# Performance work log

Hardware: AMD Instinct MI355X
Metric: run time of the kernel (lower is better)

## Reference

```python
import jax, jax.numpy as jnp
import numpy as np

B = 16384          # batch
NS = 26            # sparse features
ND = 13            # dense features
V = 100000         # vocab per sparse feature
E = 16             # embedding size
H = 400            # dnn hidden
DNN_IN = NS * E + ND  # 429


def setup_inputs() -> dict:
    key = jax.random.key(0)
    ks = jax.random.split(key, 12)
    X_sparse = jax.random.randint(ks[0], (B, NS), 0, V, dtype=jnp.int32)
    X_dense = jax.random.normal(ks[1], (B, ND), dtype=jnp.float32)
    # stacked per-feature embedding tables: [NS, V, dim]
    emb1 = jax.random.normal(ks[2], (NS, V, 1), dtype=jnp.float32) * 1e-4
    emb2 = jax.random.normal(ks[3], (NS, V, E), dtype=jnp.float32) * 1e-4
    lin_weight = jax.random.normal(ks[4], (ND, 1), dtype=jnp.float32) * 1e-4
    bias = jnp.zeros((1,), dtype=jnp.float32)
    W0 = jax.random.normal(ks[5], (DNN_IN, H), dtype=jnp.float32) * 1e-4
    b0 = jnp.zeros((H,), dtype=jnp.float32)
    W1 = jax.random.normal(ks[6], (H, H), dtype=jnp.float32) * 1e-4
    b1 = jnp.zeros((H,), dtype=jnp.float32)
    W2 = jax.random.normal(ks[7], (H, H), dtype=jnp.float32) * 1e-4
    b2 = jnp.zeros((H,), dtype=jnp.float32)
    W_out = jax.random.normal(ks[8], (H, 1), dtype=jnp.float32) * 1e-4
    return {"X_sparse": X_sparse, "X_dense": X_dense, "emb1": emb1, "emb2": emb2,
            "lin_weight": lin_weight, "bias": bias, "W0": W0, "b0": b0,
            "W1": W1, "b1": b1, "W2": W2, "b2": b2, "W_out": W_out}


def reference(X_sparse, X_dense, emb1, emb2, lin_weight, bias, W0, b0, W1, b1, W2, b2, W_out):
    fidx = jnp.arange(NS)[None, :]            # [1, NS] feature indices
    # ---- FM linear term ----
    e1 = emb1[fidx, X_sparse][..., 0]          # [B, NS] per-feature scalar embeddings
    linear_sparse = jnp.sum(e1, axis=-1, keepdims=True)            # [B, 1]
    linear_dense = X_dense @ lin_weight                            # [B, 1]
    logit = linear_sparse + linear_dense
    # ---- FM second-order cross term ----
    e2 = emb2[fidx, X_sparse]                  # [B, NS, E]
    square_of_sum = jnp.square(jnp.sum(e2, axis=1))                # [B, E]
    sum_of_square = jnp.sum(jnp.square(e2), axis=1)                # [B, E]
    cross = 0.5 * jnp.sum(square_of_sum - sum_of_square, axis=-1, keepdims=True)
    logit = logit + cross
    # ---- DNN (dropout p=0 -> identity) ----
    dnn_in = jnp.concatenate([e2.reshape(e2.shape[0], -1), X_dense], axis=-1)  # [B, 429]
    h = jax.nn.relu(dnn_in @ W0 + b0)
    h = jax.nn.relu(h @ W1 + b1)
    h = jax.nn.relu(h @ W2 + b2)
    logit = logit + h @ W_out
    return logit + bias
```

## Files before the change

### kernel.cpp

```cpp
#include <hip/hip_runtime.h>
#include <hip/hip_bf16.h>

#define B_     16384
#define NS_    26
#define ND_    13
#define V_     100000
#define E_     16
#define H_     400
#define HP     416
#define K0P    448

typedef __bf16 bf16x8 __attribute__((ext_vector_type(8)));
typedef float  f32x4  __attribute__((ext_vector_type(4)));

__device__ __forceinline__ unsigned short f2bf(float f) {
  __hip_bfloat16 h = __float2bfloat16(f);
  return __builtin_bit_cast(unsigned short, h);
}
__device__ __forceinline__ float bf2f(unsigned short u) {
  unsigned v = ((unsigned)u) << 16;
  return __builtin_bit_cast(float, v);
}

__global__ __launch_bounds__(256) void fm_kernel(
    const int* __restrict__ Xs, const float* __restrict__ Xd,
    const float* __restrict__ emb1, const float* __restrict__ emb2,
    const float* __restrict__ linw, const float* __restrict__ bias,
    unsigned short* __restrict__ dnn, float* __restrict__ out) {
  const int row  = blockIdx.x * 16 + (threadIdx.x >> 4);
  const int lane = threadIdx.x & 15;
  const int* xs = Xs + row * NS_;
  unsigned short* drow = dnn + (size_t)row * K0P;

  float s_sum = 0.f, s_sq = 0.f;
#pragma unroll
  for (int f = 0; f < NS_; ++f) {
    int idx = xs[f];
    float v = emb2[((size_t)f * V_ + idx) * E_ + lane];
    s_sum += v;
    s_sq  += v * v;
    drow[f * 16 + lane] = f2bf(v);
  }

  float lin = 0.f;
  for (int f = lane; f < NS_; f += 16)
    lin += emb1[(size_t)f * V_ + xs[f]];

  float xdv = 0.f;
  if (lane < ND_) {
    xdv = Xd[row * ND_ + lane];
    lin += xdv * linw[lane];
  }
  drow[416 + lane] = f2bf(lane < ND_ ? xdv : 0.f);
  drow[432 + lane] = 0;

  float r = 0.5f * (s_sum * s_sum - s_sq) + lin;
#pragma unroll
  for (int m = 8; m >= 1; m >>= 1) r += __shfl_xor(r, m, 64);
  if (lane == 0) out[row] = r + bias[0];
}

__global__ __launch_bounds__(256) void conv_w(
    const float* __restrict__ W, unsigned short* __restrict__ Wt, int K, int Kp) {
  int i = blockIdx.x * 256 + threadIdx.x;
  int total = Kp * HP;
  if (i >= total) return;
  int k = i / HP;
  int n = i - k * HP;
  float v = (k < K && n < H_) ? W[k * H_ + n] : 0.f;
  Wt[(size_t)n * Kp + k] = f2bf(v);
}

__global__ void pad_bias(const float* __restrict__ b, float* __restrict__ bp) {
  int i = blockIdx.x * 256 + threadIdx.x;
  if (i < HP) bp[i] = (i < H_) ? b[i] : 0.f;
}

__global__ __launch_bounds__(256) void gemm_relu(
    const unsigned short* __restrict__ A, const unsigned short* __restrict__ Bt,
    const float* __restrict__ bias, unsigned short* __restrict__ C, int K) {
  __shared__ unsigned short As[64][40];
  __shared__ unsigned short Bs[32][40];

  const int tid  = threadIdx.x;
  const int wave = tid >> 6;
  const int lane = tid & 63;
  const int quad = lane >> 4;
  const int l16  = lane & 15;
  const int rowBase = blockIdx.x * 64;
  const int colBase = blockIdx.y * 32;

  const int ar = tid >> 2, aseg = tid & 3;
  const int bn = tid >> 3, bseg = tid & 7;

  const unsigned short* aptr = A  + (size_t)(rowBase + ar) * K + aseg * 8;
  const unsigned short* bptr = Bt + (size_t)(colBase + bn) * K + bseg * 4;

  f32x4 acc0 = {0.f, 0.f, 0.f, 0.f};
  f32x4 acc1 = {0.f, 0.f, 0.f, 0.f};

  const int nK = K >> 5;
  for (int kt = 0; kt < nK; ++kt) {
    uint4 av = *(const uint4*)(aptr + kt * 32);
    uint2 bv = *(const uint2*)(bptr + kt * 32);
    __syncthreads();
    *(uint4*)&As[ar][aseg * 8] = av;
    *(uint2*)&Bs[bn][bseg * 4] = bv;
    __syncthreads();

    uint4 au  = *(const uint4*)&As[wave * 16 + l16][quad * 8];
    uint4 b0u = *(const uint4*)&Bs[l16][quad * 8];
    uint4 b1u = *(const uint4*)&Bs[16 + l16][quad * 8];
    bf16x8 af  = __builtin_bit_cast(bf16x8, au);
    bf16x8 bf0 = __builtin_bit_cast(bf16x8, b0u);
    bf16x8 bf1 = __builtin_bit_cast(bf16x8, b1u);
    acc0 = __builtin_amdgcn_mfma_f32_16x16x32_bf16(af, bf0, acc0, 0, 0, 0);
    acc1 = __builtin_amdgcn_mfma_f32_16x16x32_bf16(af, bf1, acc1, 0, 0, 0);
  }

#pragma unroll
  for (int t = 0; t < 2; ++t) {
    f32x4 a = (t == 0) ? acc0 : acc1;
    int col = colBase + t * 16 + l16;
    float bz = bias[col];
#pragma unroll
    for (int r = 0; r < 4; ++r) {
      int row = rowBase + wave * 16 + quad * 4 + r;
      float v = a[r] + bz;
      v = v > 0.f ? v : 0.f;
      C[(size_t)row * HP + col] = f2bf(v);
    }
  }
}

__global__ __launch_bounds__(256) void out_dot(
    const unsigned short* __restrict__ h2, const float* __restrict__ Wout,
    float* __restrict__ out) {
  const int row  = blockIdx.x * 4 + (threadIdx.x >> 6);
  const int lane = threadIdx.x & 63;
  const unsigned short* hr = h2 + (size_t)row * HP;
  float s = 0.f;
  for (int c = lane; c < H_; c += 64) s += bf2f(hr[c]) * Wout[c];
#pragma unroll
  for (int m = 32; m >= 1; m >>= 1) s += __shfl_xor(s, m, 64);
  if (lane == 0) out[row] += s;
}

extern "C" void kernel_launch(void* const* d_in, const int* in_sizes, int n_in,
                              void* d_out, int out_size, void* d_ws, size_t ws_size,
                              hipStream_t stream) {
  const int*   Xs   = (const int*)d_in[0];
  const float* Xd   = (const float*)d_in[1];
  const float* emb1 = (const float*)d_in[2];
  const float* emb2 = (const float*)d_in[3];
  const float* linw = (const float*)d_in[4];
  const float* bias = (const float*)d_in[5];
  const float* W0   = (const float*)d_in[6];
  const float* b0   = (const float*)d_in[7];
  const float* W1   = (const float*)d_in[8];
  const float* b1   = (const float*)d_in[9];
  const float* W2   = (const float*)d_in[10];
  const float* b2   = (const float*)d_in[11];
  const float* Wout = (const float*)d_in[12];
  float* out = (float*)d_out;

  char* ws = (char*)d_ws;
  unsigned short* P0  = (unsigned short*)(ws);
  unsigned short* P1  = (unsigned short*)(ws + 14680064);
  unsigned short* W0t = (unsigned short*)(ws + 28311552);
  unsigned short* W1t = (unsigned short*)(ws + 28684288);
  unsigned short* W2t = (unsigned short*)(ws + 29030400);
  float* b0p = (float*)(ws + 29376512);
  float* b1p = (float*)(ws + 29378176);
  float* b2p = (float*)(ws + 29379840);

  fm_kernel<<<B_ / 16, 256, 0, stream>>>(Xs, Xd, emb1, emb2, linw, bias, P0, out);

  conv_w<<<(K0P * HP + 255) / 256, 256, 0, stream>>>(W0, W0t, 429, K0P);
  conv_w<<<(HP * HP + 255) / 256, 256, 0, stream>>>(W1, W1t, 400, HP);
  conv_w<<<(HP * HP + 255) / 256, 256, 0, stream>>>(W2, W2t, 400, HP);
  pad_bias<<<2, 256, 0, stream>>>(b0, b0p);
  pad_bias<<<2, 256, 0, stream>>>(b1, b1p);
  pad_bias<<<2, 256, 0, stream>>>(b2, b2p);

  dim3 grid(B_ / 64, HP / 32);
  gemm_relu<<<grid, 256, 0, stream>>>(P0, W0t, b0p, P1, K0P);
  gemm_relu<<<grid, 256, 0, stream>>>(P1, W1t, b1p, P0, HP);
  gemm_relu<<<grid, 256, 0, stream>>>(P0, W2t, b2p, P1, HP);

  out_dot<<<B_ / 4, 256, 0, stream>>>(P1, Wout, out);
}
```

Baseline: 332.1 us.

## Enlarge GEMM tiles, prefetch operands, fuse output dot, merge weight conversion

The GEMM block tile grows from 64x32 to 128x64, with each wave computing a 32x64 sub-tile using eight MFMA accumulators, and the next k-slice is loaded from global memory into registers while the current one is computed. The last layer folds the Wout dot product into its epilogue with shuffle reductions and atomicAdd, so the final activation is never written and no separate out_dot kernel runs. The three weight conversions and the bias/Wout padding are merged into a single launch, and all padding is now 448. These changes cut launch count, global traffic and operand reloads, at the cost of more registers per thread, extra padded columns, and atomic contention on out.

```diff
diff --git a/kernel.cpp b/kernel.cpp
--- a/kernel.cpp
+++ b/kernel.cpp
@@ -7,8 +7,8 @@
 #define V_     100000
 #define E_     16
 #define H_     400
-#define HP     416
-#define K0P    448
+#define NP     448
+#define K0A    429
 
 typedef __bf16 bf16x8 __attribute__((ext_vector_type(8)));
 typedef float  f32x4  __attribute__((ext_vector_type(4)));
@@ -16,10 +16,6 @@
 __device__ __forceinline__ unsigned short f2bf(float f) {
   __hip_bfloat16 h = __float2bfloat16(f);
   return __builtin_bit_cast(unsigned short, h);
-}
-__device__ __forceinline__ float bf2f(unsigned short u) {
-  unsigned v = ((unsigned)u) << 16;
-  return __builtin_bit_cast(float, v);
 }
 
 __global__ __launch_bounds__(256) void fm_kernel(
@@ -30,7 +26,7 @@
   const int row  = blockIdx.x * 16 + (threadIdx.x >> 4);
   const int lane = threadIdx.x & 15;
   const int* xs = Xs + row * NS_;
-  unsigned short* drow = dnn + (size_t)row * K0P;
+  unsigned short* drow = dnn + (size_t)row * NP;
 
   float s_sum = 0.f, s_sq = 0.f;
 #pragma unroll
@@ -60,90 +56,124 @@
   if (lane == 0) out[row] = r + bias[0];
 }
 
-__global__ __launch_bounds__(256) void conv_w(
-    const float* __restrict__ W, unsigned short* __restrict__ Wt, int K, int Kp) {
+__global__ __launch_bounds__(256) void conv_all(
+    const float* __restrict__ W0, const float* __restrict__ W1,
+    const float* __restrict__ W2, const float* __restrict__ b0,
+    const float* __restrict__ b1, const float* __restrict__ b2,
+    const float* __restrict__ Wout,
+    unsigned short* __restrict__ W0t, unsigned short* __restrict__ W1t,
+    unsigned short* __restrict__ W2t, float* __restrict__ b0p,
+    float* __restrict__ b1p, float* __restrict__ b2p,
+    float* __restrict__ woutp) {
+  const int WSZ = NP * NP;
   int i = blockIdx.x * 256 + threadIdx.x;
-  int total = Kp * HP;
-  if (i >= total) return;
-  int k = i / HP;
-  int n = i - k * HP;
-  float v = (k < K && n < H_) ? W[k * H_ + n] : 0.f;
-  Wt[(size_t)n * Kp + k] = f2bf(v);
-}
-
-__global__ void pad_bias(const float* __restrict__ b, float* __restrict__ bp) {
-  int i = blockIdx.x * 256 + threadIdx.x;
-  if (i < HP) bp[i] = (i < H_) ? b[i] : 0.f;
+  if (i < 3 * WSZ) {
+    int which = i / WSZ;
+    int j = i - which * WSZ;
+    int k = j / NP, n = j - (j / NP) * NP;
+    const float* W = (which == 0) ? W0 : (which == 1) ? W1 : W2;
+    unsigned short* Wt = (which == 0) ? W0t : (which == 1) ? W1t : W2t;
+    int Kact = (which == 0) ? K0A : H_;
+    float v = (k < Kact && n < H_) ? W[k * H_ + n] : 0.f;
+    Wt[(size_t)n * NP + k] = f2bf(v);
+  } else {
+    int j = i - 3 * WSZ;
+    if (j < NP)          b0p[j]            = (j < H_) ? b0[j] : 0.f;
+    else if (j < 2 * NP) b1p[j - NP]       = (j - NP < H_) ? b1[j - NP] : 0.f;
+    else if (j < 3 * NP) b2p[j - 2 * NP]   = (j - 2 * NP < H_) ? b2[j - 2 * NP] : 0.f;
+    else if (j < 4 * NP) woutp[j - 3 * NP] = (j - 3 * NP < H_) ? Wout[j - 3 * NP] : 0.f;
+  }
 }
 
 __global__ __launch_bounds__(256) void gemm_relu(
     const unsigned short* __restrict__ A, const unsigned short* __restrict__ Bt,
-    const float* __restrict__ bias, unsigned short* __restrict__ C, int K) {
-  __shared__ unsigned short As[64][40];
-  __shared__ unsigned short Bs[32][40];
+    const float* __restrict__ bias, unsigned short* __restrict__ C,
+    const float* __restrict__ wout, float* __restrict__ out, int fuse) {
+  __shared__ unsigned short As[128][40];
+  __shared__ unsigned short Bs[64][40];
 
   const int tid  = threadIdx.x;
   const int wave = tid >> 6;
   const int lane = tid & 63;
   const int quad = lane >> 4;
   const int l16  = lane & 15;
-  const int rowBase = blockIdx.x * 64;
-  const int colBase = blockIdx.y * 32;
-
-  const int ar = tid >> 2, aseg = tid & 3;
-  const int bn = tid >> 3, bseg = tid & 7;
-
-  const unsigned short* aptr = A  + (size_t)(rowBase + ar) * K + aseg * 8;
-  const unsigned short* bptr = Bt + (size_t)(colBase + bn) * K + bseg * 4;
-
-  f32x4 acc0 = {0.f, 0.f, 0.f, 0.f};
-  f32x4 acc1 = {0.f, 0.f, 0.f, 0.f};
-
-  const int nK = K >> 5;
+  const int rowBase = blockIdx.x * 128;
+  const int colBase = blockIdx.y * 64;
+
+  const int sr = tid >> 2, sseg = tid & 3;
+  const unsigned short* aptr0 = A  + (size_t)(rowBase + sr) * NP + sseg * 8;
+  const unsigned short* aptr1 = A  + (size_t)(rowBase + 64 + sr) * NP + sseg * 8;
+  const unsigned short* bptr  = Bt + (size_t)(colBase + sr) * NP + sseg * 8;
+
+  f32x4 acc[2][4] = {};
+
+  uint4 a0 = *(const uint4*)(aptr0);
+  uint4 a1 = *(const uint4*)(aptr1);
+  uint4 bv = *(const uint4*)(bptr);
+
+  const int nK = NP / 32;
   for (int kt = 0; kt < nK; ++kt) {
-    uint4 av = *(const uint4*)(aptr + kt * 32);
-    uint2 bv = *(const uint2*)(bptr + kt * 32);
     __syncthreads();
-    *(uint4*)&As[ar][aseg * 8] = av;
-    *(uint2*)&Bs[bn][bseg * 4] = bv;
+    *(uint4*)&As[sr][sseg * 8]      = a0;
+    *(uint4*)&As[64 + sr][sseg * 8] = a1;
+    *(uint4*)&Bs[sr][sseg * 8]      = bv;
     __syncthreads();
 
-    uint4 au  = *(const uint4*)&As[wave * 16 + l16][quad * 8];
-    uint4 b0u = *(const uint4*)&Bs[l16][quad * 8];
-    uint4 b1u = *(const uint4*)&Bs[16 + l16][quad * 8];
-    bf16x8 af  = __builtin_bit_cast(bf16x8, au);
-    bf16x8 bf0 = __builtin_bit_cast(bf16x8, b0u);
-    bf16x8 bf1 = __builtin_bit_cast(bf16x8, b1u);
-    acc0 = __builtin_amdgcn_mfma_f32_16x16x32_bf16(af, bf0, acc0, 0, 0, 0);
-    acc1 = __builtin_amdgcn_mfma_f32_16x16x32_bf16(af, bf1, acc1, 0, 0, 0);
-  }
-
-#pragma unroll
-  for (int t = 0; t < 2; ++t) {
-    f32x4 a = (t == 0) ? acc0 : acc1;
-    int col = colBase + t * 16 + l16;
-    float bz = bias[col];
-#pragma unroll
-    for (int r = 0; r < 4; ++r) {
-      int row = rowBase + wave * 16 + quad * 4 + r;
-      float v = a[r] + bz;
-      v = v > 0.f ? v : 0.f;
-      C[(size_t)row * HP + col] = f2bf(v);
-    }
-  }
-}
-
-__global__ __launch_bounds__(256) void out_dot(
-    const unsigned short* __restrict__ h2, const float* __restrict__ Wout,
-    float* __restrict__ out) {
-  const int row  = blockIdx.x * 4 + (threadIdx.x >> 6);
-  const int lane = threadIdx.x & 63;
-  const unsigned short* hr = h2 + (size_t)row * HP;
-  float s = 0.f;
-  for (int c = lane; c < H_; c += 64) s += bf2f(hr[c]) * Wout[c];
-#pragma unroll
-  for (int m = 32; m >= 1; m >>= 1) s += __shfl_xor(s, m, 64);
-  if (lane == 0) out[row] += s;
+    if (kt + 1 < nK) {
+      a0 = *(const uint4*)(aptr0 + (kt + 1) * 32);
+      a1 = *(const uint4*)(aptr1 + (kt + 1) * 32);
+      bv = *(const uint4*)(bptr + (kt + 1) * 32);
+    }
+
+    bf16x8 af0 = __builtin_bit_cast(bf16x8, *(const uint4*)&As[wave * 32 + l16][quad * 8]);
+    bf16x8 af1 = __builtin_bit_cast(bf16x8, *(const uint4*)&As[wave * 32 + 16 + l16][quad * 8]);
+#pragma unroll
+    for (int nt = 0; nt < 4; ++nt) {
+      bf16x8 bf = __builtin_bit_cast(bf16x8, *(const uint4*)&Bs[nt * 16 + l16][quad * 8]);
+      acc[0][nt] = __builtin_amdgcn_mfma_f32_16x16x32_bf16(af0, bf, acc[0][nt], 0, 0, 0);
+      acc[1][nt] = __builtin_amdgcn_mfma_f32_16x16x32_bf16(af1, bf, acc[1][nt], 0, 0, 0);
+    }
+  }
+
+  float wsum[2][4] = {};
+#pragma unroll
+  for (int mt = 0; mt < 2; ++mt) {
+#pragma unroll
+    for (int nt = 0; nt < 4; ++nt) {
+      int col = colBase + nt * 16 + l16;
+      float bz = bias[col];
+      float wv = wout[col];
+#pragma unroll
+      for (int r = 0; r < 4; ++r) {
+        float v = acc[mt][nt][r] + bz;
+        v = v > 0.f ? v : 0.f;
+        if (!fuse) {
+          int row = rowBase + wave * 32 + mt * 16 + quad * 4 + r;
+          C[(size_t)row * NP + col] = f2bf(v);
+        } else {
+          wsum[mt][r] += v * wv;
+        }
+      }
+    }
+  }
+
+  if (fuse) {
+#pragma unroll
+    for (int mt = 0; mt < 2; ++mt) {
+#pragma unroll
+      for (int r = 0; r < 4; ++r) {
+        float s = wsum[mt][r];
+        s += __shfl_xor(s, 1, 64);
+        s += __shfl_xor(s, 2, 64);
+        s += __shfl_xor(s, 4, 64);
+        s += __shfl_xor(s, 8, 64);
+        if (l16 == 0) {
+          int row = rowBase + wave * 32 + mt * 16 + quad * 4 + r;
+          atomicAdd(out + row, s);
+        }
+      }
+    }
+  }
 }
 
 extern "C" void kernel_launch(void* const* d_in, const int* in_sizes, int n_in,
@@ -165,28 +195,25 @@
   float* out = (float*)d_out;
 
   char* ws = (char*)d_ws;
+  const size_t PSZ = (size_t)B_ * NP * 2;
+  const size_t WSZ = (size_t)NP * NP * 2;
   unsigned short* P0  = (unsigned short*)(ws);
-  unsigned short* P1  = (unsigned short*)(ws + 14680064);
-  unsigned short* W0t = (unsigned short*)(ws + 28311552);
-  unsigned short* W1t = (unsigned short*)(ws + 28684288);
-  unsigned short* W2t = (unsigned short*)(ws + 29030400);
-  float* b0p = (float*)(ws + 29376512);
-  float* b1p = (float*)(ws + 29378176);
-  float* b2p = (float*)(ws + 29379840);
+  unsigned short* P1  = (unsigned short*)(ws + PSZ);
+  unsigned short* W0t = (unsigned short*)(ws + 2 * PSZ);
+  unsigned short* W1t = (unsigned short*)(ws + 2 * PSZ + WSZ);
+  unsigned short* W2t = (unsigned short*)(ws + 2 * PSZ + 2 * WSZ);
+  float* b0p   = (float*)(ws + 2 * PSZ + 3 * WSZ);
+  float* b1p   = (float*)(ws + 2 * PSZ + 3 * WSZ + 1792);
+  float* b2p   = (float*)(ws + 2 * PSZ + 3 * WSZ + 2 * 1792);
+  float* woutp = (float*)(ws + 2 * PSZ + 3 * WSZ + 3 * 1792);
 
   fm_kernel<<<B_ / 16, 256, 0, stream>>>(Xs, Xd, emb1, emb2, linw, bias, P0, out);
 
-  conv_w<<<(K0P * HP + 255) / 256, 256, 0, stream>>>(W0, W0t, 429, K0P);
-  conv_w<<<(HP * HP + 255) / 256, 256, 0, stream>>>(W1, W1t, 400, HP);
-  conv_w<<<(HP * HP + 255) / 256, 256, 0, stream>>>(W2, W2t, 400, HP);
-  pad_bias<<<2, 256, 0, stream>>>(b0, b0p);
-  pad_bias<<<2, 256, 0, stream>>>(b1, b1p);
-  pad_bias<<<2, 256, 0, stream>>>(b2, b2p);
-
-  dim3 grid(B_ / 64, HP / 32);
-  gemm_relu<<<grid, 256, 0, stream>>>(P0, W0t, b0p, P1, K0P);
-  gemm_relu<<<grid, 256, 0, stream>>>(P1, W1t, b1p, P0, HP);
-  gemm_relu<<<grid, 256, 0, stream>>>(P0, W2t, b2p, P1, HP);
-
-  out_dot<<<B_ / 4, 256, 0, stream>>>(P1, Wout, out);
-}
+  conv_all<<<(3 * NP * NP + 4 * NP) / 256, 256, 0, stream>>>(
+      W0, W1, W2, b0, b1, b2, Wout, W0t, W1t, W2t, b0p, b1p, b2p, woutp);
+
+  dim3 grid(B_ / 128, NP / 64);
+  gemm_relu<<<grid, 256, 0, stream>>>(P0, W0t, b0p, P1, woutp, out, 0);
+  gemm_relu<<<grid, 256, 0, stream>>>(P1, W1t, b1p, P0, woutp, out, 0);
+  gemm_relu<<<grid, 256, 0, stream>>>(P0, W2t, b2p, P1, woutp, out, 1);
+}
```

Measured after the change: 297.0 us. 10.6% less time.
